# Performance work log

Hardware: AMD Instinct MI355X
Metric: run time of the kernel (lower is better)

Reference implementation:

```python
import jax, jax.numpy as jnp
import numpy as np

NUM_BITS = 4
BLOCK = 64
IN_F = 4096
OUT_F = 4096
RANK = 16


def dequantize(packed_qweight, weight_max, lookup_table):
    """Unpack sub-byte indices from uint8 bytes, lookup codebook, apply per-block absmax scale.
    packed_qweight: [n_bytes, 1] uint8; weight_max: [n_blocks]; lookup_table: [2**NUM_BITS].
    Returns dequantized weight [OUT_F, IN_F]."""
    nipb = 8 // NUM_BITS  # indices per byte
    mask = (1 << NUM_BITS) - 1
    b = packed_qweight[:, 0]
    # index i was packed at bit position i*NUM_BITS (LSB first)
    idx = jnp.stack([(b >> (i * NUM_BITS)) & mask for i in range(nipb)], axis=-1).reshape(-1)
    w = lookup_table[idx].reshape(-1, BLOCK) * weight_max[:, None]  # [n_blocks, BLOCK]
    return w.reshape(OUT_F, IN_F)


def setup_inputs() -> dict:
    key = jax.random.key(0)
    k0, k1, k2, k3, k4, k5 = jax.random.split(key, 6)
    x = jax.random.normal(k0, (4, 2048, IN_F), dtype=jnp.float32)
    packed_qweight = jax.random.randint(k1, (OUT_F * IN_F // (8 // NUM_BITS), 1), 0, 256, dtype=jnp.int32).astype(jnp.uint8)
    weight_max = jax.random.uniform(k2, (OUT_F * IN_F // BLOCK,), dtype=jnp.float32, minval=0.01, maxval=0.1)
    # uniform non-symmetric codebook: linspace(-1, 1, 2**num_bits)
    lookup_table = jnp.linspace(-1.0, 1.0, 2 ** NUM_BITS, dtype=jnp.float32)
    lora_A = jax.random.normal(k3, (RANK, IN_F), dtype=jnp.float32) * 0.02
    lora_B = jax.random.normal(k4, (OUT_F, RANK), dtype=jnp.float32) * 0.02
    bias = jax.random.normal(k5, (OUT_F,), dtype=jnp.float32) * 0.02
    return {"x": x, "packed_qweight": packed_qweight, "weight_max": weight_max,
            "lookup_table": lookup_table, "lora_A": lora_A, "lora_B": lora_B, "bias": bias}


def reference(x, packed_qweight, weight_max, lookup_table, lora_A, lora_B, bias):
    W = dequantize(packed_qweight, weight_max, lookup_table)  # [OUT_F, IN_F]
    base = jnp.einsum('bsi,oi->bso', x, W)
    lora = jnp.einsum('bsr,or->bso', jnp.einsum('bsi,ri->bsr', x, lora_A), lora_B)
    return base + lora + bias
```

## Files before the change

### kernel.cpp

```cpp
#include <hip/hip_runtime.h>
#include <hip/hip_bf16.h>
#include <stdint.h>

constexpr int IN_F  = 4096;
constexpr int OUT_F = 4096;
constexpr int M_ROWS = 4 * 2048;
constexpr int RANK = 16;

typedef short short8 __attribute__((ext_vector_type(8)));
typedef float f32x4 __attribute__((ext_vector_type(4)));

__device__ __forceinline__ short f2bf(float f) {
  return __builtin_bit_cast(short, __float2bfloat16(f));
}

__device__ __forceinline__ void gload16(const void* g, void* l) {
  __builtin_amdgcn_global_load_lds(
      (const __attribute__((address_space(1))) void*)g,
      (__attribute__((address_space(3))) void*)l, 16, 0, 0);
}

__global__ __launch_bounds__(256) void prep_kernel(
    const int* __restrict__ q,
    const float* __restrict__ wmax,
    const float* __restrict__ lut,
    const float* __restrict__ lA,
    const float* __restrict__ lB,
    const float* __restrict__ x,
    __hip_bfloat16* __restrict__ W,
    __hip_bfloat16* __restrict__ xb) {
  if (blockIdx.x < 512) {
    __shared__ float slut[16];
    if (threadIdx.x < 16) slut[threadIdx.x] = lut[threadIdx.x];
    __syncthreads();

    const int bx = blockIdx.x & 7, by = blockIdx.x >> 3;
    const int o0  = by * 64 + (threadIdx.x >> 5) * 8;
    const int ib0 = bx * 512 + (threadIdx.x & 31) * 16;

    #pragma unroll
    for (int h = 0; h < 2; ++h) {
      const int ib = ib0 + h * 8;
      float w[8][8];
      #pragma unroll
      for (int p = 0; p < 8; ++p) {
        const size_t l = (size_t)(o0 + p) * IN_F + ib;
        const int4 u = *(const int4*)(q + (l >> 1));
        const float sc = wmax[l >> 6];
        w[p][0] = slut[u.x & 15] * sc;
        w[p][1] = slut[(u.x >> 4) & 15] * sc;
        w[p][2] = slut[u.y & 15] * sc;
        w[p][3] = slut[(u.y >> 4) & 15] * sc;
        w[p][4] = slut[u.z & 15] * sc;
        w[p][5] = slut[(u.z >> 4) & 15] * sc;
        w[p][6] = slut[u.w & 15] * sc;
        w[p][7] = slut[(u.w >> 4) & 15] * sc;
      }
      #pragma unroll 2
      for (int r = 0; r < 16; ++r) {
        const float* ar = lA + (size_t)r * IN_F + ib;
        const float4 a0 = *(const float4*)(ar);
        const float4 a1 = *(const float4*)(ar + 4);
        float b[8];
        #pragma unroll
        for (int p = 0; p < 8; ++p) b[p] = lB[(size_t)(o0 + p) * RANK + r];
        #pragma unroll
        for (int p = 0; p < 8; ++p) {
          w[p][0] += b[p] * a0.x; w[p][1] += b[p] * a0.y;
          w[p][2] += b[p] * a0.z; w[p][3] += b[p] * a0.w;
          w[p][4] += b[p] * a1.x; w[p][5] += b[p] * a1.y;
          w[p][6] += b[p] * a1.z; w[p][7] += b[p] * a1.w;
        }
      }
      #pragma unroll
      for (int p = 0; p < 8; ++p) {
        short8 s;
        #pragma unroll
        for (int qq = 0; qq < 8; ++qq) s[qq] = f2bf(w[p][qq]);
        *(short8*)&W[(size_t)(o0 + p) * IN_F + ib] = s;
      }
    }
  } else {
    constexpr int NG = (M_ROWS * IN_F) / 8;
    const int stride = 2048 * 256;
    for (int i = (blockIdx.x - 512) * 256 + threadIdx.x; i < NG; i += stride) {
      const float4 a = ((const float4*)x)[2 * i];
      const float4 b = ((const float4*)x)[2 * i + 1];
      short8 s;
      s[0] = f2bf(a.x); s[1] = f2bf(a.y); s[2] = f2bf(a.z); s[3] = f2bf(a.w);
      s[4] = f2bf(b.x); s[5] = f2bf(b.y); s[6] = f2bf(b.z); s[7] = f2bf(b.w);
      ((short8*)xb)[i] = s;
    }
  }
}

constexpr int BM = 256, BN = 256, BK = 64;
constexpr int GM = M_ROWS, GN = OUT_F, GK = IN_F;
constexpr int NKT = GK / BK;

#define LOAD_B(BUF, KH)                                                   \
  _Pragma("unroll")                                                       \
  for (int n_ = 0; n_ < 4; ++n_)                                          \
    bf[n_] = *(const short8*)&sB[BUF][KH][wn * 64 + n_ * 16 + lr][swr * 8];

#define LOAD_A(BUF, KH, MH)                                               \
  _Pragma("unroll")                                                       \
  for (int i_ = 0; i_ < 4; ++i_)                                          \
    af[i_] = *(const short8*)&sA[BUF][KH][wm * 128 + (MH) * 64 + i_ * 16 + lr][swr * 8];

#define MFMA_Q(MH)                                                        \
  __builtin_amdgcn_s_setprio(1);                                          \
  _Pragma("unroll")                                                       \
  for (int i_ = 0; i_ < 4; ++i_)                                          \
    _Pragma("unroll")                                                     \
    for (int n_ = 0; n_ < 4; ++n_)                                        \
      acc[(MH) * 4 + i_][n_] = __builtin_amdgcn_mfma_f32_16x16x32_bf16(   \
          af[i_], bf[n_], acc[(MH) * 4 + i_][n_], 0, 0, 0);               \
  __builtin_amdgcn_s_setprio(0);

#define PHASE(BUF, KH, MH, DOB, GB, LB, VM)                               \
  do {                                                                    \
    if (DOB) { LOAD_B(BUF, KH) }                                          \
    LOAD_A(BUF, KH, MH)                                                   \
    stage(GB, LB);                                                        \
    if (VM) asm volatile("s_waitcnt vmcnt(6)" ::: "memory");              \
    __builtin_amdgcn_s_barrier();                                         \
    MFMA_Q(MH)                                                            \
    __builtin_amdgcn_sched_barrier(0);                                    \
    __builtin_amdgcn_s_barrier();                                         \
  } while (0)

__global__ __launch_bounds__(512, 2) void gemm_bt_final(
    const __hip_bfloat16* __restrict__ A,
    const __hip_bfloat16* __restrict__ B,
    const float* __restrict__ bias,
    float* __restrict__ C) {
  __shared__ __hip_bfloat16 sA[2][2][256][32];
  __shared__ __hip_bfloat16 sB[2][2][256][32];

  const int tid  = threadIdx.x;
  const int lane = tid & 63;
  const int wave = tid >> 6;
  const int lr = lane & 15;
  const int lk = lane >> 4;
  const int wm = wave >> 2;
  const int wn = wave & 3;
  const int swr = lk ^ ((lr >> 1) & 3);

  const int bid = blockIdx.x;
  const int cpx = gridDim.x >> 3;
  const int wg  = (bid & 7) * cpx + (bid >> 3);
  const int nbn = GN / BN;
  const int m0 = (wg / nbn) * BM;
  const int n0 = (wg % nbn) * BN;

  const __hip_bfloat16* Abase = A + (size_t)m0 * GK;
  const __hip_bfloat16* Bbase = B + (size_t)n0 * GK;

  const int swst = (tid >> 3) & 3;
  auto stage = [&](const __hip_bfloat16* gb, __hip_bfloat16* lb) {
    #pragma unroll
    for (int j = 0; j < 2; ++j) {
      const int c = j * 512 + tid;
      const int row = c >> 2, slot = c & 3;
      const int sg = slot ^ swst;
      gload16(gb + (size_t)row * GK + sg * 8,
              (void*)((char*)lb + (j * 512 + wave * 64) * 16));
    }
  };

  f32x4 acc[8][4];
  #pragma unroll
  for (int m = 0; m < 8; ++m)
    #pragma unroll
    for (int n = 0; n < 4; ++n) acc[m][n] = (f32x4)0.0f;

  stage(Abase +  0, &sA[0][0][0][0]);
  stage(Bbase +  0, &sB[0][0][0][0]);
  stage(Abase + 32, &sA[0][1][0][0]);
  stage(Bbase + 32, &sB[0][1][0][0]);
  stage(Bbase + 64, &sB[1][0][0][0]);
  stage(Abase + 64, &sA[1][0][0][0]);
  stage(Bbase + 96, &sB[1][1][0][0]);
  asm volatile("s_waitcnt vmcnt(6)" ::: "memory");
  __builtin_amdgcn_s_barrier();

  short8 af[4], bf[4];

  for (int t = 0; t < NKT; t += 2) {
    const int t2 = (t + 2 < NKT) ? t + 2 : NKT - 1;
    const int t3 = (t + 3 < NKT) ? t + 3 : NKT - 1;

    PHASE(0, 0, 0, true,  Abase + (size_t)(t + 1) * 64 + 32, &sA[1][1][0][0], false);
    PHASE(0, 0, 1, false, Bbase + (size_t)t2 * 64,           &sB[0][0][0][0], false);
    PHASE(0, 1, 0, true,  Abase + (size_t)t2 * 64,           &sA[0][0][0][0], false);
    PHASE(0, 1, 1, false, Bbase + (size_t)t2 * 64 + 32,      &sB[0][1][0][0], true);
    PHASE(1, 0, 0, true,  Abase + (size_t)t2 * 64 + 32,      &sA[0][1][0][0], false);
    PHASE(1, 0, 1, false, Bbase + (size_t)t3 * 64,           &sB[1][0][0][0], false);
    PHASE(1, 1, 0, true,  Abase + (size_t)t3 * 64,           &sA[1][0][0][0], false);
    PHASE(1, 1, 1, false, Bbase + (size_t)t3 * 64 + 32,      &sB[1][1][0][0], true);
  }

  #pragma unroll
  for (int n = 0; n < 4; ++n) {
    const int col = n0 + wn * 64 + n * 16 + lr;
    const float bv = bias[col];
    #pragma unroll
    for (int m = 0; m < 8; ++m) {
      const int row = m0 + wm * 128 + m * 16 + lk * 4;
      #pragma unroll
      for (int j = 0; j < 4; ++j)
        __builtin_nontemporal_store(acc[m][n][j] + bv,
                                    &C[(size_t)(row + j) * GN + col]);
    }
  }
}

extern "C" void kernel_launch(void* const* d_in, const int* in_sizes, int n_in,
                              void* d_out, int out_size, void* d_ws, size_t ws_size,
                              hipStream_t stream) {
  const float* x    = (const float*)d_in[0];
  const int*   qw   = (const int*)d_in[1];
  const float* wmax = (const float*)d_in[2];
  const float* lut  = (const float*)d_in[3];
  const float* lA   = (const float*)d_in[4];
  const float* lB   = (const float*)d_in[5];
  const float* bias = (const float*)d_in[6];
  float* out = (float*)d_out;

  __hip_bfloat16* Weff = (__hip_bfloat16*)d_ws;
  __hip_bfloat16* xb   = (__hip_bfloat16*)((char*)d_ws + (size_t)OUT_F * IN_F * 2);

  prep_kernel<<<2560, 256, 0, stream>>>(qw, wmax, lut, lA, lB, x, Weff, xb);
  gemm_bt_final<<<(GM / BM) * (GN / BN), 512, 0, stream>>>(xb, Weff, bias, out);
}
```

Baseline: 315.1 us.

## Double-buffer LDS fragment reads to overlap with MFMA and drop a barrier

Each phase of the GEMM main loop now issues the LDS reads for the next phase's A/B fragments into a second register set before running the current MFMAs. Only a partial lgkmcnt wait is used, so LDS latency overlaps with matrix math. The second per-phase barrier is removed to cut synchronization stalls. This adds register pressure from the doubled fragment buffers and relies on the stage ordering to avoid LDS write-after-read hazards.

```diff
diff --git a/kernel.cpp b/kernel.cpp
--- a/kernel.cpp
+++ b/kernel.cpp
@@ -98,39 +98,39 @@
 constexpr int GM = M_ROWS, GN = OUT_F, GK = IN_F;
 constexpr int NKT = GK / BK;
 
-#define LOAD_B(BUF, KH)                                                   \
+#define LOAD_Bn(RB_, RKH, DST)                                            \
   _Pragma("unroll")                                                       \
   for (int n_ = 0; n_ < 4; ++n_)                                          \
-    bf[n_] = *(const short8*)&sB[BUF][KH][wn * 64 + n_ * 16 + lr][swr * 8];
-
-#define LOAD_A(BUF, KH, MH)                                               \
+    bfr[DST][n_] = *(const short8*)&sB[RB_][RKH][wn * 64 + n_ * 16 + lr][swr * 8];
+
+#define LOAD_An(RB_, RKH, RMH, DST)                                       \
   _Pragma("unroll")                                                       \
   for (int i_ = 0; i_ < 4; ++i_)                                          \
-    af[i_] = *(const short8*)&sA[BUF][KH][wm * 128 + (MH) * 64 + i_ * 16 + lr][swr * 8];
-
-#define MFMA_Q(MH)                                                        \
+    afr[DST][i_] = *(const short8*)&sA[RB_][RKH][wm * 128 + (RMH) * 64 + i_ * 16 + lr][swr * 8];
+
+#define MFMA_Q(CMH, AC, BC)                                               \
   __builtin_amdgcn_s_setprio(1);                                          \
   _Pragma("unroll")                                                       \
   for (int i_ = 0; i_ < 4; ++i_)                                          \
     _Pragma("unroll")                                                     \
     for (int n_ = 0; n_ < 4; ++n_)                                        \
-      acc[(MH) * 4 + i_][n_] = __builtin_amdgcn_mfma_f32_16x16x32_bf16(   \
-          af[i_], bf[n_], acc[(MH) * 4 + i_][n_], 0, 0, 0);               \
+      acc[(CMH) * 4 + i_][n_] = __builtin_amdgcn_mfma_f32_16x16x32_bf16(  \
+          afr[AC][i_], bfr[BC][n_], acc[(CMH) * 4 + i_][n_], 0, 0, 0);    \
   __builtin_amdgcn_s_setprio(0);
 
-#define PHASE(BUF, KH, MH, DOB, GB, LB, VM)                               \
+#define PHASE(AC, BC, NDOB, NBUF, NKH, NMH, CMH, GB, LB, VM, NLG)         \
   do {                                                                    \
-    if (DOB) { LOAD_B(BUF, KH) }                                          \
-    LOAD_A(BUF, KH, MH)                                                   \
     stage(GB, LB);                                                        \
     if (VM) asm volatile("s_waitcnt vmcnt(6)" ::: "memory");              \
     __builtin_amdgcn_s_barrier();                                         \
-    MFMA_Q(MH)                                                            \
+    if (NDOB) { LOAD_Bn(NBUF, NKH, (BC) ^ 1) }                            \
+    LOAD_An(NBUF, NKH, NMH, (AC) ^ 1)                                     \
+    asm volatile("s_waitcnt lgkmcnt(" #NLG ")" ::: "memory");             \
     __builtin_amdgcn_sched_barrier(0);                                    \
-    __builtin_amdgcn_s_barrier();                                         \
+    MFMA_Q(CMH, AC, BC)                                                   \
   } while (0)
 
-__global__ __launch_bounds__(512, 2) void gemm_bt_final(
+__global__ __launch_bounds__(512, 2) void gemm_bt_ovl(
     const __hip_bfloat16* __restrict__ A,
     const __hip_bfloat16* __restrict__ B,
     const float* __restrict__ bias,
@@ -185,20 +185,22 @@
   asm volatile("s_waitcnt vmcnt(6)" ::: "memory");
   __builtin_amdgcn_s_barrier();
 
-  short8 af[4], bf[4];
+  short8 afr[2][4], bfr[2][4];
+  LOAD_Bn(0, 0, 0)
+  LOAD_An(0, 0, 0, 1)
 
   for (int t = 0; t < NKT; t += 2) {
     const int t2 = (t + 2 < NKT) ? t + 2 : NKT - 1;
     const int t3 = (t + 3 < NKT) ? t + 3 : NKT - 1;
 
-    PHASE(0, 0, 0, true,  Abase + (size_t)(t + 1) * 64 + 32, &sA[1][1][0][0], false);
-    PHASE(0, 0, 1, false, Bbase + (size_t)t2 * 64,           &sB[0][0][0][0], false);
-    PHASE(0, 1, 0, true,  Abase + (size_t)t2 * 64,           &sA[0][0][0][0], false);
-    PHASE(0, 1, 1, false, Bbase + (size_t)t2 * 64 + 32,      &sB[0][1][0][0], true);
-    PHASE(1, 0, 0, true,  Abase + (size_t)t2 * 64 + 32,      &sA[0][1][0][0], false);
-    PHASE(1, 0, 1, false, Bbase + (size_t)t3 * 64,           &sB[1][0][0][0], false);
-    PHASE(1, 1, 0, true,  Abase + (size_t)t3 * 64,           &sA[1][0][0][0], false);
-    PHASE(1, 1, 1, false, Bbase + (size_t)t3 * 64 + 32,      &sB[1][1][0][0], true);
+    PHASE(1, 0, 0, 0, 0, 1, 0,  Abase + (size_t)(t + 1) * 64 + 32, &sA[1][1][0][0], 0, 4);
+    PHASE(0, 0, 1, 0, 1, 0, 1,  Bbase + (size_t)t2 * 64,           &sB[0][0][0][0], 0, 8);
+    PHASE(1, 1, 0, 0, 1, 1, 0,  Abase + (size_t)t2 * 64,           &sA[0][0][0][0], 0, 4);
+    PHASE(0, 1, 1, 1, 0, 0, 1,  Bbase + (size_t)t2 * 64 + 32,      &sB[0][1][0][0], 1, 8);
+    PHASE(1, 0, 0, 1, 0, 1, 0,  Abase + (size_t)t2 * 64 + 32,      &sA[0][1][0][0], 0, 4);
+    PHASE(0, 0, 1, 1, 1, 0, 1,  Bbase + (size_t)t3 * 64,           &sB[1][0][0][0], 0, 8);
+    PHASE(1, 1, 0, 1, 1, 1, 0,  Abase + (size_t)t3 * 64,           &sA[1][0][0][0], 0, 4);
+    PHASE(0, 1, 1, 0, 0, 0, 1,  Bbase + (size_t)t3 * 64 + 32,      &sB[1][1][0][0], 1, 8);
   }
 
   #pragma unroll
@@ -232,5 +234,5 @@
   __hip_bfloat16* xb   = (__hip_bfloat16*)((char*)d_ws + (size_t)OUT_F * IN_F * 2);
 
   prep_kernel<<<2560, 256, 0, stream>>>(qw, wmax, lut, lA, lB, x, Weff, xb);
-  gemm_bt_final<<<(GM / BM) * (GN / BN), 512, 0, stream>>>(xb, Weff, bias, out);
-}
+  gemm_bt_ovl<<<(GM / BM) * (GN / BN), 512, 0, stream>>>(xb, Weff, bias, out);
+}
```

After: 302.1 us. 1.04x faster.

## Merge GEMM phases and double-buffer LDS fragments in registers

Applied to the files above, without the earlier changes.

Restructures the main loop from eight half-phases into four full k-half phases. Each phase now stages both A and B tiles, issues one barrier, and prefetches the next A/B fragments from LDS into a second register buffer while the MFMAs run on the current one. The aim is fewer barriers per K step and LDS reads hidden behind matrix math. In exchange it needs more VGPRs for fragments (afr/bfr doubled), which risks spills or reduced occupancy at 512x2 launch bounds, and the waitcnt counts must stay correct.

```diff
diff --git a/kernel.cpp b/kernel.cpp
--- a/kernel.cpp
+++ b/kernel.cpp
@@ -98,39 +98,41 @@
 constexpr int GM = M_ROWS, GN = OUT_F, GK = IN_F;
 constexpr int NKT = GK / BK;
 
-#define LOAD_B(BUF, KH)                                                   \
+#define LOAD_AB(RB_, RKH, DST)                                            \
   _Pragma("unroll")                                                       \
   for (int n_ = 0; n_ < 4; ++n_)                                          \
-    bf[n_] = *(const short8*)&sB[BUF][KH][wn * 64 + n_ * 16 + lr][swr * 8];
-
-#define LOAD_A(BUF, KH, MH)                                               \
+    bfr[DST][n_] = *(const short8*)&sB[RB_][RKH][wn * 64 + n_ * 16 + lr][swr * 8]; \
   _Pragma("unroll")                                                       \
-  for (int i_ = 0; i_ < 4; ++i_)                                          \
-    af[i_] = *(const short8*)&sA[BUF][KH][wm * 128 + (MH) * 64 + i_ * 16 + lr][swr * 8];
-
-#define MFMA_Q(MH)                                                        \
+  for (int mh_ = 0; mh_ < 2; ++mh_)                                       \
+    _Pragma("unroll")                                                     \
+    for (int i_ = 0; i_ < 4; ++i_)                                        \
+      afr[DST][mh_ * 4 + i_] = *(const short8*)&sA[RB_][RKH][wm * 128 + mh_ * 64 + i_ * 16 + lr][swr * 8];
+
+#define MFMA_P(CUR)                                                       \
   __builtin_amdgcn_s_setprio(1);                                          \
   _Pragma("unroll")                                                       \
-  for (int i_ = 0; i_ < 4; ++i_)                                          \
+  for (int mh_ = 0; mh_ < 2; ++mh_)                                       \
     _Pragma("unroll")                                                     \
-    for (int n_ = 0; n_ < 4; ++n_)                                        \
-      acc[(MH) * 4 + i_][n_] = __builtin_amdgcn_mfma_f32_16x16x32_bf16(   \
-          af[i_], bf[n_], acc[(MH) * 4 + i_][n_], 0, 0, 0);               \
+    for (int i_ = 0; i_ < 4; ++i_)                                        \
+      _Pragma("unroll")                                                   \
+      for (int n_ = 0; n_ < 4; ++n_)                                      \
+        acc[mh_ * 4 + i_][n_] = __builtin_amdgcn_mfma_f32_16x16x32_bf16(  \
+            afr[CUR][mh_ * 4 + i_], bfr[CUR][n_], acc[mh_ * 4 + i_][n_], 0, 0, 0); \
   __builtin_amdgcn_s_setprio(0);
 
-#define PHASE(BUF, KH, MH, DOB, GB, LB, VM)                               \
+#define PHASE(CUR, SB, SK, GOFF, NB, NK)                                  \
   do {                                                                    \
-    if (DOB) { LOAD_B(BUF, KH) }                                          \
-    LOAD_A(BUF, KH, MH)                                                   \
-    stage(GB, LB);                                                        \
-    if (VM) asm volatile("s_waitcnt vmcnt(6)" ::: "memory");              \
+    stage(Abase + (GOFF), &sA[SB][SK][0][0]);                             \
+    stage(Bbase + (GOFF), &sB[SB][SK][0][0]);                             \
+    asm volatile("s_waitcnt vmcnt(8)" ::: "memory");                      \
     __builtin_amdgcn_s_barrier();                                         \
-    MFMA_Q(MH)                                                            \
+    LOAD_AB(NB, NK, (CUR) ^ 1)                                            \
+    asm volatile("s_waitcnt lgkmcnt(12)" ::: "memory");                   \
     __builtin_amdgcn_sched_barrier(0);                                    \
-    __builtin_amdgcn_s_barrier();                                         \
+    MFMA_P(CUR)                                                           \
   } while (0)
 
-__global__ __launch_bounds__(512, 2) void gemm_bt_final(
+__global__ __launch_bounds__(512, 2) void gemm_bt_mrg2(
     const __hip_bfloat16* __restrict__ A,
     const __hip_bfloat16* __restrict__ B,
     const float* __restrict__ bias,
@@ -179,26 +181,22 @@
   stage(Bbase +  0, &sB[0][0][0][0]);
   stage(Abase + 32, &sA[0][1][0][0]);
   stage(Bbase + 32, &sB[0][1][0][0]);
+  stage(Abase + 64, &sA[1][0][0][0]);
   stage(Bbase + 64, &sB[1][0][0][0]);
-  stage(Abase + 64, &sA[1][0][0][0]);
-  stage(Bbase + 96, &sB[1][1][0][0]);
-  asm volatile("s_waitcnt vmcnt(6)" ::: "memory");
+  asm volatile("s_waitcnt vmcnt(4)" ::: "memory");
   __builtin_amdgcn_s_barrier();
 
-  short8 af[4], bf[4];
+  short8 afr[2][8], bfr[2][4];
+  LOAD_AB(0, 0, 0)
 
   for (int t = 0; t < NKT; t += 2) {
     const int t2 = (t + 2 < NKT) ? t + 2 : NKT - 1;
     const int t3 = (t + 3 < NKT) ? t + 3 : NKT - 1;
 
-    PHASE(0, 0, 0, true,  Abase + (size_t)(t + 1) * 64 + 32, &sA[1][1][0][0], false);
-    PHASE(0, 0, 1, false, Bbase + (size_t)t2 * 64,           &sB[0][0][0][0], false);
-    PHASE(0, 1, 0, true,  Abase + (size_t)t2 * 64,           &sA[0][0][0][0], false);
-    PHASE(0, 1, 1, false, Bbase + (size_t)t2 * 64 + 32,      &sB[0][1][0][0], true);
-    PHASE(1, 0, 0, true,  Abase + (size_t)t2 * 64 + 32,      &sA[0][1][0][0], false);
-    PHASE(1, 0, 1, false, Bbase + (size_t)t3 * 64,           &sB[1][0][0][0], false);
-    PHASE(1, 1, 0, true,  Abase + (size_t)t3 * 64,           &sA[1][0][0][0], false);
-    PHASE(1, 1, 1, false, Bbase + (size_t)t3 * 64 + 32,      &sB[1][1][0][0], true);
+    PHASE(0,  1, 1,  (size_t)(t + 1) * 64 + 32,    0, 1);
+    PHASE(1,  0, 0,  (size_t)t2 * 64,              1, 0);
+    PHASE(0,  0, 1,  (size_t)t2 * 64 + 32,         1, 1);
+    PHASE(1,  1, 0,  (size_t)t3 * 64,              0, 0);
   }
 
   #pragma unroll
@@ -232,5 +230,5 @@
   __hip_bfloat16* xb   = (__hip_bfloat16*)((char*)d_ws + (size_t)OUT_F * IN_F * 2);
 
   prep_kernel<<<2560, 256, 0, stream>>>(qw, wmax, lut, lA, lB, x, Weff, xb);
-  gemm_bt_final<<<(GM / BM) * (GN / BN), 512, 0, stream>>>(xb, Weff, bias, out);
-}
+  gemm_bt_mrg2<<<(GM / BM) * (GN / BN), 512, 0, stream>>>(xb, Weff, bias, out);
+}
```

Measured after the change: 302.5 us. 4.0% less time.
